# Kernel tuning notes

Measured on AMD Instinct MI355X. Metric: run time of the kernel, lower is better.

## Reference

```python
import jax, jax.numpy as jnp
from jax import lax
import numpy as np

N = 256              # total neurons
EPG_LO, EPG_HI = 0, 64      # epg population slice
PEN_LO, PEN_HI = 64, 128    # pen population slice (two hemispheres of 32)
HEMI = 32                    # hemisphere_length_penalty = len(pen)/2
T = 512              # Euler integration steps
B = 1024             # batch of independent trajectories
DT = 0.01            # integration step (seconds)
TAU0 = 0.02          # default time constant (seconds)


def setup_inputs() -> dict:
    key = jax.random.key(0)
    k_w, k_v, k_l = jax.random.split(key, 3)
    W = jax.random.normal(k_w, (N, N), dtype=jnp.float32) * 0.1
    log_scale = jnp.zeros((), dtype=jnp.float32)          # exp(0)=1, initial_weight_scale=1.0
    gain = jnp.ones((N,), dtype=jnp.float32)              # per-neuron gain mask (exp of per-pop params)
    bias = jnp.zeros((N,), dtype=jnp.float32)
    log_tau = jnp.full((N,), np.log(TAU0), dtype=jnp.float32)  # exp -> tau = 0.02
    velocity_scaling = jnp.float32(0.1)
    landmark_scaling = jnp.float32(0.1)
    velocity = jax.random.normal(k_v, (T, B, 2), dtype=jnp.float32)
    landmarks = jax.random.uniform(k_l, (T, B, EPG_HI - EPG_LO), dtype=jnp.float32)
    return {"W": W, "log_scale": log_scale, "gain": gain, "bias": bias,
            "log_tau": log_tau, "velocity_scaling": velocity_scaling,
            "landmark_scaling": landmark_scaling, "velocity": velocity,
            "landmarks": landmarks}


def reference(W, log_scale, gain, bias, log_tau, velocity_scaling,
              landmark_scaling, velocity, landmarks):
    # Effective recurrent weights: sum over blocks of exp(scale)*masked block
    # collapses to exp(log_scale) * W when all block scalings are tied.
    W_eff = jnp.exp(log_scale) * W                      # [N, N]
    tau = jnp.exp(log_tau)                              # [N]
    coef = DT / tau                                     # [N] Euler dt/tau

    def step(state, xs):                                # state: [B, N]
        v, lm = xs                                      # v: [B, 2], lm: [B, 64]
        ext = jnp.zeros((B, N), dtype=state.dtype)
        # landmark input -> epg neurons
        ext = ext.at[:, EPG_LO:EPG_HI].set(lm * landmark_scaling)
        # angular velocity -> pen neurons, split by hemisphere
        ext = ext.at[:, PEN_LO:PEN_LO + HEMI].set(v[:, :1] * velocity_scaling)
        ext = ext.at[:, PEN_LO + HEMI:PEN_HI].set(v[:, 1:2] * velocity_scaling)
        total = state @ W_eff + ext                     # [B, N]
        rate = jax.nn.relu(gain * total + bias)
        new_state = state + coef * (rate - state)       # leaky Euler update
        return new_state, None

    state0 = jnp.zeros((B, N), dtype=jnp.float32)
    final, _ = lax.scan(step, state0, (velocity, landmarks))
    return final[:, EPG_LO:EPG_HI]                      # epg output, [B, 64]
```

## Files before the change

### kernel.cpp

```cpp
#include <hip/hip_runtime.h>

#define NN 256
#define TT 512
#define BB 1024
#define DTC 0.01f

typedef _Float16 half8 __attribute__((ext_vector_type(8)));
typedef float f32x4 __attribute__((ext_vector_type(4)));
typedef float f32x2 __attribute__((ext_vector_type(2)));

__device__ __forceinline__ f32x4 mfma_z(half8 a, half8 b) {
  f32x4 d;
  asm volatile("v_mfma_f32_16x16x32_f16 %0, %1, %2, 0" : "=v"(d) : "a"(a), "v"(b));
  return d;
}
__device__ __forceinline__ void mfma_p(f32x4& c, half8 a, half8 b) {
  asm volatile("v_mfma_f32_16x16x32_f16 %0, %1, %2, %0" : "+v"(c) : "a"(a), "v"(b));
}

template <int CTRL>
__device__ __forceinline__ float rormax(float x) {
  int yi = __builtin_amdgcn_update_dpp(0, __float_as_int(x), CTRL, 0xf, 0xf, false);
  return fmaxf(x, __int_as_float(yi));
}

__global__ __launch_bounds__(256, 1) void ring_attractor_kernel(
    const float* __restrict__ W, const float* __restrict__ log_scale,
    const float* __restrict__ gain, const float* __restrict__ bias,
    const float* __restrict__ log_tau, const float* __restrict__ vscale_p,
    const float* __restrict__ lscale_p, const float* __restrict__ velocity,
    const float* __restrict__ landmarks, float* __restrict__ out) {
  __shared__ __align__(16) _Float16 fragH[2][4096];
  __shared__ __align__(16) _Float16 fragL[2][4096];
  __shared__ __align__(16) float maxslot[2][4];

  const int tid = threadIdx.x;
  const int w  = tid >> 6;
  const int l  = tid & 63;
  const int g  = l >> 4;
  const int li = l & 15;
  const int br = blockIdx.x * 16 + li;

  const float es  = expf(log_scale[0]);
  const float vs  = vscale_p[0];
  const float lms = lscale_p[0];

  float gain_r[4][4], bias_r[4][4], coef_r[4][4];
#pragma unroll
  for (int nt = 0; nt < 4; ++nt)
#pragma unroll
    for (int q = 0; q < 4; ++q) {
      int c = w * 64 + nt * 16 + g * 4 + q;
      gain_r[nt][q] = gain[c];
      bias_r[nt][q] = bias[c];
      coef_r[nt][q] = DTC / expf(log_tau[c]);
    }

  half8 whi[4][8], wlo[4][8];
#pragma unroll
  for (int nt = 0; nt < 4; ++nt)
#pragma unroll
    for (int ks = 0; ks < 8; ++ks) {
      half8 hi, lo;
#pragma unroll
      for (int j = 0; j < 8; ++j) {
        int k = ks * 32 + g * 4 + (j & 3) + ((j >> 2) << 4);
        int m = w * 64 + nt * 16 + li;
        float wv = W[k * NN + m] * es;
        _Float16 h = (_Float16)wv;
        hi[j] = h;
        lo[j] = (_Float16)(wv - (float)h);
      }
      whi[nt][ks] = hi;
      wlo[nt][ks] = lo;
    }

  float s_r[4][4];
#pragma unroll
  for (int nt = 0; nt < 4; ++nt)
#pragma unroll
    for (int q = 0; q < 4; ++q) s_r[nt][q] = 0.f;

  const int wb0 = ((w * 2 + 0) * 64 + g * 16 + li) * 8;
  const int wb1 = ((w * 2 + 1) * 64 + g * 16 + li) * 8;
  {
    half8 z;
#pragma unroll
    for (int j = 0; j < 8; ++j) z[j] = (_Float16)0.f;
    *reinterpret_cast<half8*>(&fragH[0][wb0]) = z;
    *reinterpret_cast<half8*>(&fragH[0][wb1]) = z;
    *reinterpret_cast<half8*>(&fragL[0][wb0]) = z;
    *reinterpret_cast<half8*>(&fragL[0][wb1]) = z;
    if (tid < 8) maxslot[tid >> 2][tid & 3] = 0.f;
  }
  float inv_scale = 1.f;
  float amPrev = 0.f;
  __syncthreads();

#define RD2(CUR, KS, BH, BL)                                                   \
  {                                                                            \
    const int rb = ((KS)*64 + g * 16 + li) * 8;                                \
    BH = *reinterpret_cast<const half8*>(&fragH[CUR][rb]);                     \
    BL = *reinterpret_cast<const half8*>(&fragL[CUR][rb]);                     \
  }

#define M3Z(AH, AL, AC, NT, BH, BL)                                            \
  AH = mfma_z(whi[NT][0], BH);                                                 \
  AL = mfma_z(wlo[NT][0], BH);                                                 \
  AC = mfma_z(whi[NT][0], BL);

#define M3(AH, AL, AC, NT, KS, BH, BL)                                         \
  mfma_p(AH, whi[NT][KS], BH);                                                 \
  mfma_p(AL, wlo[NT][KS], BH);                                                 \
  mfma_p(AC, whi[NT][KS], BL);

#define TIE0(AH, AL, AC) \
  asm volatile("" : "+v"(AH), "+v"(AL), "+v"(AC))
#define TIEN(AH, AL, AC) \
  asm volatile("s_nop 7\n\ts_nop 7" : "+v"(AH), "+v"(AL), "+v"(AC))

#define TQ(NT, Q, AH, AL, AC)                                                  \
  {                                                                            \
    float av = AH[Q] + AL[Q] + AC[Q];                                          \
    float ext;                                                                 \
    if (w == 0)                                                                \
      ext = lms * ((NT == 0)   ? lm0[Q]                                        \
                   : (NT == 1) ? lm1[Q]                                        \
                   : (NT == 2) ? lm2[Q]                                        \
                               : lm3[Q]);                                      \
    else if (w == 1)                                                           \
      ext = vs * ((NT < 2) ? vv0 : vv1);                                       \
    else                                                                       \
      ext = 0.f;                                                               \
    float tot = __builtin_fmaf(av, inv_scale, ext);                            \
    float rate =                                                               \
        fmaxf(__builtin_fmaf(gain_r[NT][Q], tot, bias_r[NT][Q]), 0.f);         \
    float sv = s_r[NT][Q];                                                     \
    sv = __builtin_fmaf(coef_r[NT][Q], rate - sv, sv);                         \
    s_r[NT][Q] = sv;                                                           \
    am = fmaxf(am, fabsf(sv));                                                 \
  }

#define QHALF(CUR, NTA, NTB, WBX)                                              \
  {                                                                            \
    half8 hq, lq;                                                              \
    _Pragma("unroll") for (int j = 0; j < 4; ++j) {                            \
      float sca = s_r[NTA][j] * scale_n;                                       \
      float scb = s_r[NTB][j] * scale_n;                                       \
      _Float16 qa = (_Float16)sca;                                             \
      _Float16 qb = (_Float16)scb;                                             \
      hq[j] = qa;                                                              \
      lq[j] = (_Float16)(sca - (float)qa);                                     \
      hq[4 + j] = qb;                                                          \
      lq[4 + j] = (_Float16)(scb - (float)qb);                                 \
    }                                                                          \
    *reinterpret_cast<half8*>(&fragH[CUR ^ 1][WBX]) = hq;                      \
    *reinterpret_cast<half8*>(&fragL[CUR ^ 1][WBX]) = lq;                      \
  }

#define STEP(T, CUR)                                                           \
  {                                                                            \
             \
    f32x4 lm0{}, lm1{}, lm2{}, lm3{};                                          \
    float vv0 = 0.f, vv1 = 0.f;                                                \
    if (w == 0) {                                                              \
      const float* p = landmarks + ((size_t)(T)*BB + br) * 64 + g * 4;         \
      lm0 = *reinterpret_cast<const f32x4*>(p);                                \
      lm1 = *reinterpret_cast<const f32x4*>(p + 16);                           \
      lm2 = *reinterpret_cast<const f32x4*>(p + 32);                           \
      lm3 = *reinterpret_cast<const f32x4*>(p + 48);                           \
    } else if (w == 1) {                                                       \
      f32x2 pv = *reinterpret_cast<const f32x2*>(velocity +                    \
                                                 ((size_t)(T)*BB + br) * 2);   \
      vv0 = pv[0];                                                             \
      vv1 = pv[1];                                                             \
    }                                                                          \
                \
    f32x4 mv = *reinterpret_cast<const f32x4*>(&maxslot[CUR ^ 1][0]);          \
                       \
    {                                                                          \
      float r = amPrev;                                                        \
      r = rormax<0x121>(r);                                                    \
      r = rormax<0x122>(r);                                                    \
      r = rormax<0x124>(r);                                                    \
      r = rormax<0x128>(r);                                                    \
      r = fmaxf(r, __shfl_xor(r, 16));                                         \
      r = fmaxf(r, __shfl_xor(r, 32));                                         \
      if (l == 0) maxslot[CUR][w] = r;                                         \
    }                                                                          \
    float scale_n, inv_n;                                                      \
    {                                                                          \
      float M = fmaxf(fmaxf(mv[0], mv[1]), fmaxf(mv[2], mv[3]));               \
      int e = 134 - (int)(__float_as_uint(M) >> 23);                           \
      e = e > 9 ? 9 : e;                                                       \
      scale_n = __int_as_float((e + 127) << 23);                               \
      inv_n = __int_as_float((127 - e) << 23);                                 \
    }                                                                          \
    half8 bh0, bl0, bh1, bl1, bh2, bl2, bh3, bl3;                              \
    half8 bh4, bl4, bh5, bl5, bh6, bl6, bh7, bl7;                              \
    RD2(CUR, 0, bh0, bl0)                                                      \
    RD2(CUR, 1, bh1, bl1)                                                      \
    RD2(CUR, 2, bh2, bl2)                                                      \
    RD2(CUR, 3, bh3, bl3)                                                      \
    RD2(CUR, 4, bh4, bl4)                                                      \
    RD2(CUR, 5, bh5, bl5)                                                      \
    RD2(CUR, 6, bh6, bl6)                                                      \
    RD2(CUR, 7, bh7, bl7)                                                      \
    f32x4 a0h, a0l, a0c, a1h, a1l, a1c, a2h, a2l, a2c, a3h, a3l, a3c;          \
    float am = 0.f;                                                            \
                                                \
    M3Z(a0h, a0l, a0c, 0, bh0, bl0)                                            \
    M3(a0h, a0l, a0c, 0, 1, bh1, bl1)                                          \
    M3(a0h, a0l, a0c, 0, 2, bh2, bl2)                                          \
    M3(a0h, a0l, a0c, 0, 3, bh3, bl3)                                          \
    M3(a0h, a0l, a0c, 0, 4, bh4, bl4)                                          \
    M3(a0h, a0l, a0c, 0, 5, bh5, bl5)                                          \
    M3(a0h, a0l, a0c, 0, 6, bh6, bl6)                                          \
    M3(a0h, a0l, a0c, 0, 7, bh7, bl7)                                          \
         \
    M3Z(a1h, a1l, a1c, 1, bh0, bl0)                                            \
    M3(a1h, a1l, a1c, 1, 1, bh1, bl1)                                          \
    TIE0(a0h, a0l, a0c);                                                       \
    TQ(0, 0, a0h, a0l, a0c)                                                    \
    M3(a1h, a1l, a1c, 1, 2, bh2, bl2)                                          \
    M3(a1h, a1l, a1c, 1, 3, bh3, bl3)                                          \
    TQ(0, 1, a0h, a0l, a0c)                                                    \
    M3(a1h, a1l, a1c, 1, 4, bh4, bl4)                                          \
    M3(a1h, a1l, a1c, 1, 5, bh5, bl5)                                          \
    TQ(0, 2, a0h, a0l, a0c)                                                    \
    M3(a1h, a1l, a1c, 1, 6, bh6, bl6)                                          \
    M3(a1h, a1l, a1c, 1, 7, bh7, bl7)                                          \
    TQ(0, 3, a0h, a0l, a0c)                                                    \
                                          \
    M3Z(a2h, a2l, a2c, 2, bh0, bl0)                                            \
    M3(a2h, a2l, a2c, 2, 1, bh1, bl1)                                          \
    TIE0(a1h, a1l, a1c);                                                       \
    TQ(1, 0, a1h, a1l, a1c)                                                    \
    M3(a2h, a2l, a2c, 2, 2, bh2, bl2)                                          \
    M3(a2h, a2l, a2c, 2, 3, bh3, bl3)                                          \
    TQ(1, 1, a1h, a1l, a1c)                                                    \
    M3(a2h, a2l, a2c, 2, 4, bh4, bl4)                                          \
    M3(a2h, a2l, a2c, 2, 5, bh5, bl5)                                          \
    TQ(1, 2, a1h, a1l, a1c)                                                    \
    M3(a2h, a2l, a2c, 2, 6, bh6, bl6)                                          \
    M3(a2h, a2l, a2c, 2, 7, bh7, bl7)                                          \
    TQ(1, 3, a1h, a1l, a1c)                                                    \
                    \
    M3Z(a3h, a3l, a3c, 3, bh0, bl0)                                            \
    M3(a3h, a3l, a3c, 3, 1, bh1, bl1)                                          \
    QHALF(CUR, 0, 1, wb0)                                                      \
    M3(a3h, a3l, a3c, 3, 2, bh2, bl2)                                          \
    M3(a3h, a3l, a3c, 3, 3, bh3, bl3)                                          \
    TIE0(a2h, a2l, a2c);                                                       \
    TQ(2, 0, a2h, a2l, a2c)                                                    \
    M3(a3h, a3l, a3c, 3, 4, bh4, bl4)                                          \
    M3(a3h, a3l, a3c, 3, 5, bh5, bl5)                                          \
    TQ(2, 1, a2h, a2l, a2c)                                                    \
    M3(a3h, a3l, a3c, 3, 6, bh6, bl6)                                          \
    M3(a3h, a3l, a3c, 3, 7, bh7, bl7)                                          \
    TQ(2, 2, a2h, a2l, a2c)                                                    \
         \
    TQ(2, 3, a2h, a2l, a2c)                                                    \
    TIEN(a3h, a3l, a3c);                                                       \
    TQ(3, 0, a3h, a3l, a3c)                                                    \
    TQ(3, 1, a3h, a3l, a3c)                                                    \
    TQ(3, 2, a3h, a3l, a3c)                                                    \
    TQ(3, 3, a3h, a3l, a3c)                                                    \
    QHALF(CUR, 2, 3, wb1)                                                      \
    amPrev = am;                                                               \
    inv_scale = inv_n;                                                         \
    __syncthreads();                                                           \
  }

#pragma unroll 1
  for (int t = 0; t < TT; t += 2) {
    STEP(t, 0)
    STEP(t + 1, 1)
  }
#undef STEP
#undef QHALF
#undef TQ
#undef TIE0
#undef TIEN
#undef M3
#undef M3Z
#undef RD2

  if (w == 0) {
#pragma unroll
    for (int nt = 0; nt < 4; ++nt) {
      f32x4 o;
#pragma unroll
      for (int q = 0; q < 4; ++q) o[q] = s_r[nt][q];
      *reinterpret_cast<f32x4*>(out + (size_t)br * 64 + nt * 16 + g * 4) = o;
    }
  }
}

extern "C" void kernel_launch(void* const* d_in, const int* in_sizes, int n_in,
                              void* d_out, int out_size, void* d_ws, size_t ws_size,
                              hipStream_t stream) {
  const float* W         = (const float*)d_in[0];
  const float* log_scale = (const float*)d_in[1];
  const float* gain      = (const float*)d_in[2];
  const float* bias      = (const float*)d_in[3];
  const float* log_tau   = (const float*)d_in[4];
  const float* vscale    = (const float*)d_in[5];
  const float* lscale    = (const float*)d_in[6];
  const float* velocity  = (const float*)d_in[7];
  const float* landmarks = (const float*)d_in[8];
  float* out = (float*)d_out;

  ring_attractor_kernel<<<dim3(BB / 16), dim3(256), 0, stream>>>(
      W, log_scale, gain, bias, log_tau, vscale, lscale, velocity, landmarks, out);
}
```

Measured before the change: 794.7 us.

## Split neuron columns across eight waves per block with interleaved MFMA schedule

Doubles the block to 512 threads so each of eight wavefronts owns 32 output neurons instead of 64. This halves per-wave weight registers and MFMA chain length per time step. The MFMA sequence now interleaves the two column tiles with the LDS fragment reads, separated by scheduling barriers. The aim is to shorten the serial per-step critical path in the recurrent loop, at the cost of more waves contending at the per-step barrier and a larger max-reduction slot array.

```diff
diff --git a/kernel.cpp b/kernel.cpp
--- a/kernel.cpp
+++ b/kernel.cpp
@@ -24,7 +24,7 @@
   return fmaxf(x, __int_as_float(yi));
 }
 
-__global__ __launch_bounds__(256, 1) void ring_attractor_kernel(
+__global__ __launch_bounds__(512, 2) void ring_attractor_kernel(
     const float* __restrict__ W, const float* __restrict__ log_scale,
     const float* __restrict__ gain, const float* __restrict__ bias,
     const float* __restrict__ log_tau, const float* __restrict__ vscale_p,
@@ -32,7 +32,7 @@
     const float* __restrict__ landmarks, float* __restrict__ out) {
   __shared__ __align__(16) _Float16 fragH[2][4096];
   __shared__ __align__(16) _Float16 fragL[2][4096];
-  __shared__ __align__(16) float maxslot[2][4];
+  __shared__ __align__(16) float maxslot[2][8];
 
   const int tid = threadIdx.x;
   const int w  = tid >> 6;
@@ -45,27 +45,27 @@
   const float vs  = vscale_p[0];
   const float lms = lscale_p[0];
 
-  float gain_r[4][4], bias_r[4][4], coef_r[4][4];
-#pragma unroll
-  for (int nt = 0; nt < 4; ++nt)
+  float gain_r[2][4], bias_r[2][4], coef_r[2][4];
+#pragma unroll
+  for (int nt = 0; nt < 2; ++nt)
 #pragma unroll
     for (int q = 0; q < 4; ++q) {
-      int c = w * 64 + nt * 16 + g * 4 + q;
+      int c = w * 32 + nt * 16 + g * 4 + q;
       gain_r[nt][q] = gain[c];
       bias_r[nt][q] = bias[c];
       coef_r[nt][q] = DTC / expf(log_tau[c]);
     }
 
-  half8 whi[4][8], wlo[4][8];
-#pragma unroll
-  for (int nt = 0; nt < 4; ++nt)
+  half8 whi[2][8], wlo[2][8];
+#pragma unroll
+  for (int nt = 0; nt < 2; ++nt)
 #pragma unroll
     for (int ks = 0; ks < 8; ++ks) {
       half8 hi, lo;
 #pragma unroll
       for (int j = 0; j < 8; ++j) {
         int k = ks * 32 + g * 4 + (j & 3) + ((j >> 2) << 4);
-        int m = w * 64 + nt * 16 + li;
+        int m = w * 32 + nt * 16 + li;
         float wv = W[k * NN + m] * es;
         _Float16 h = (_Float16)wv;
         hi[j] = h;
@@ -75,27 +75,26 @@
       wlo[nt][ks] = lo;
     }
 
-  float s_r[4][4];
-#pragma unroll
-  for (int nt = 0; nt < 4; ++nt)
+  float s_r[2][4];
+#pragma unroll
+  for (int nt = 0; nt < 2; ++nt)
 #pragma unroll
     for (int q = 0; q < 4; ++q) s_r[nt][q] = 0.f;
 
-  const int wb0 = ((w * 2 + 0) * 64 + g * 16 + li) * 8;
-  const int wb1 = ((w * 2 + 1) * 64 + g * 16 + li) * 8;
+  const int wb = (w * 64 + g * 16 + li) * 8;
   {
     half8 z;
 #pragma unroll
     for (int j = 0; j < 8; ++j) z[j] = (_Float16)0.f;
-    *reinterpret_cast<half8*>(&fragH[0][wb0]) = z;
-    *reinterpret_cast<half8*>(&fragH[0][wb1]) = z;
-    *reinterpret_cast<half8*>(&fragL[0][wb0]) = z;
-    *reinterpret_cast<half8*>(&fragL[0][wb1]) = z;
-    if (tid < 8) maxslot[tid >> 2][tid & 3] = 0.f;
+    *reinterpret_cast<half8*>(&fragH[0][wb]) = z;
+    *reinterpret_cast<half8*>(&fragL[0][wb]) = z;
+    if (tid < 16) maxslot[tid >> 3][tid & 7] = 0.f;
   }
   float inv_scale = 1.f;
   float amPrev = 0.f;
   __syncthreads();
+
+#define SB() __builtin_amdgcn_sched_barrier(0)
 
 #define RD2(CUR, KS, BH, BL)                                                   \
   {                                                                            \
@@ -104,18 +103,21 @@
     BL = *reinterpret_cast<const half8*>(&fragL[CUR][rb]);                     \
   }
 
-#define M3Z(AH, AL, AC, NT, BH, BL)                                            \
-  AH = mfma_z(whi[NT][0], BH);                                                 \
-  AL = mfma_z(wlo[NT][0], BH);                                                 \
-  AC = mfma_z(whi[NT][0], BL);
-
-#define M3(AH, AL, AC, NT, KS, BH, BL)                                         \
-  mfma_p(AH, whi[NT][KS], BH);                                                 \
-  mfma_p(AL, wlo[NT][KS], BH);                                                 \
-  mfma_p(AC, whi[NT][KS], BL);
-
-#define TIE0(AH, AL, AC) \
-  asm volatile("" : "+v"(AH), "+v"(AL), "+v"(AC))
+#define K6Z(BH, BL)                                                            \
+  a0h = mfma_z(whi[0][0], BH);                                                 \
+  a1h = mfma_z(whi[1][0], BH);                                                 \
+  a0l = mfma_z(wlo[0][0], BH);                                                 \
+  a1l = mfma_z(wlo[1][0], BH);                                                 \
+  a0c = mfma_z(whi[0][0], BL);                                                 \
+  a1c = mfma_z(whi[1][0], BL);
+#define K6(KS, BH, BL)                                                         \
+  mfma_p(a0h, whi[0][KS], BH);                                                 \
+  mfma_p(a1h, whi[1][KS], BH);                                                 \
+  mfma_p(a0l, wlo[0][KS], BH);                                                 \
+  mfma_p(a1l, wlo[1][KS], BH);                                                 \
+  mfma_p(a0c, whi[0][KS], BL);                                                 \
+  mfma_p(a1c, whi[1][KS], BL);
+
 #define TIEN(AH, AL, AC) \
   asm volatile("s_nop 7\n\ts_nop 7" : "+v"(AH), "+v"(AL), "+v"(AC))
 
@@ -123,13 +125,12 @@
   {                                                                            \
     float av = AH[Q] + AL[Q] + AC[Q];                                          \
     float ext;                                                                 \
-    if (w == 0)                                                                \
-      ext = lms * ((NT == 0)   ? lm0[Q]                                        \
-                   : (NT == 1) ? lm1[Q]                                        \
-                   : (NT == 2) ? lm2[Q]                                        \
-                               : lm3[Q]);                                      \
-    else if (w == 1)                                                           \
-      ext = vs * ((NT < 2) ? vv0 : vv1);                                       \
+    if (w < 2)                                                                 \
+      ext = lms * ((NT) ? lm1[Q] : lm0[Q]);                                    \
+    else if (w == 2)                                                           \
+      ext = vs * vv0;                                                          \
+    else if (w == 3)                                                           \
+      ext = vs * vv1;                                                          \
     else                                                                       \
       ext = 0.f;                                                               \
     float tot = __builtin_fmaf(av, inv_scale, ext);                            \
@@ -141,43 +142,24 @@
     am = fmaxf(am, fabsf(sv));                                                 \
   }
 
-#define QHALF(CUR, NTA, NTB, WBX)                                              \
-  {                                                                            \
-    half8 hq, lq;                                                              \
-    _Pragma("unroll") for (int j = 0; j < 4; ++j) {                            \
-      float sca = s_r[NTA][j] * scale_n;                                       \
-      float scb = s_r[NTB][j] * scale_n;                                       \
-      _Float16 qa = (_Float16)sca;                                             \
-      _Float16 qb = (_Float16)scb;                                             \
-      hq[j] = qa;                                                              \
-      lq[j] = (_Float16)(sca - (float)qa);                                     \
-      hq[4 + j] = qb;                                                          \
-      lq[4 + j] = (_Float16)(scb - (float)qb);                                 \
-    }                                                                          \
-    *reinterpret_cast<half8*>(&fragH[CUR ^ 1][WBX]) = hq;                      \
-    *reinterpret_cast<half8*>(&fragL[CUR ^ 1][WBX]) = lq;                      \
-  }
-
 #define STEP(T, CUR)                                                           \
   {                                                                            \
-             \
-    f32x4 lm0{}, lm1{}, lm2{}, lm3{};                                          \
+                           \
+    f32x4 lm0{}, lm1{};                                                        \
     float vv0 = 0.f, vv1 = 0.f;                                                \
-    if (w == 0) {                                                              \
-      const float* p = landmarks + ((size_t)(T)*BB + br) * 64 + g * 4;         \
+    if (w < 2) {                                                               \
+      const float* p = landmarks + ((size_t)(T)*BB + br) * 64 + w * 32 + g * 4;\
       lm0 = *reinterpret_cast<const f32x4*>(p);                                \
       lm1 = *reinterpret_cast<const f32x4*>(p + 16);                           \
-      lm2 = *reinterpret_cast<const f32x4*>(p + 32);                           \
-      lm3 = *reinterpret_cast<const f32x4*>(p + 48);                           \
-    } else if (w == 1) {                                                       \
+    } else if (w < 4) {                                                        \
       f32x2 pv = *reinterpret_cast<const f32x2*>(velocity +                    \
                                                  ((size_t)(T)*BB + br) * 2);   \
       vv0 = pv[0];                                                             \
       vv1 = pv[1];                                                             \
     }                                                                          \
-                \
-    f32x4 mv = *reinterpret_cast<const f32x4*>(&maxslot[CUR ^ 1][0]);          \
-                       \
+                 \
+    f32x4 mva = *reinterpret_cast<const f32x4*>(&maxslot[CUR ^ 1][0]);         \
+    f32x4 mvb = *reinterpret_cast<const f32x4*>(&maxslot[CUR ^ 1][4]);         \
     {                                                                          \
       float r = amPrev;                                                        \
       r = rormax<0x121>(r);                                                    \
@@ -190,83 +172,70 @@
     }                                                                          \
     float scale_n, inv_n;                                                      \
     {                                                                          \
-      float M = fmaxf(fmaxf(mv[0], mv[1]), fmaxf(mv[2], mv[3]));               \
+      float M = fmaxf(fmaxf(fmaxf(mva[0], mva[1]), fmaxf(mva[2], mva[3])),     \
+                      fmaxf(fmaxf(mvb[0], mvb[1]), fmaxf(mvb[2], mvb[3])));    \
       int e = 134 - (int)(__float_as_uint(M) >> 23);                           \
       e = e > 9 ? 9 : e;                                                       \
       scale_n = __int_as_float((e + 127) << 23);                               \
       inv_n = __int_as_float((127 - e) << 23);                                 \
     }                                                                          \
+                   \
     half8 bh0, bl0, bh1, bl1, bh2, bl2, bh3, bl3;                              \
     half8 bh4, bl4, bh5, bl5, bh6, bl6, bh7, bl7;                              \
+    f32x4 a0h, a0l, a0c, a1h, a1l, a1c;                                        \
     RD2(CUR, 0, bh0, bl0)                                                      \
     RD2(CUR, 1, bh1, bl1)                                                      \
+    SB();                                                                      \
+    K6Z(bh0, bl0)                                                              \
+    SB();                                                                      \
     RD2(CUR, 2, bh2, bl2)                                                      \
+    SB();                                                                      \
+    K6(1, bh1, bl1)                                                            \
+    SB();                                                                      \
     RD2(CUR, 3, bh3, bl3)                                                      \
+    SB();                                                                      \
+    K6(2, bh2, bl2)                                                            \
+    SB();                                                                      \
     RD2(CUR, 4, bh4, bl4)                                                      \
+    SB();                                                                      \
+    K6(3, bh3, bl3)                                                            \
+    SB();                                                                      \
     RD2(CUR, 5, bh5, bl5)                                                      \
+    SB();                                                                      \
+    K6(4, bh4, bl4)                                                            \
+    SB();                                                                      \
     RD2(CUR, 6, bh6, bl6)                                                      \
+    SB();                                                                      \
+    K6(5, bh5, bl5)                                                            \
+    SB();                                                                      \
     RD2(CUR, 7, bh7, bl7)                                                      \
-    f32x4 a0h, a0l, a0c, a1h, a1l, a1c, a2h, a2l, a2c, a3h, a3l, a3c;          \
+    SB();                                                                      \
+    K6(6, bh6, bl6)                                                            \
+    K6(7, bh7, bl7)                                                            \
+              \
     float am = 0.f;                                                            \
-                                                \
-    M3Z(a0h, a0l, a0c, 0, bh0, bl0)                                            \
-    M3(a0h, a0l, a0c, 0, 1, bh1, bl1)                                          \
-    M3(a0h, a0l, a0c, 0, 2, bh2, bl2)                                          \
-    M3(a0h, a0l, a0c, 0, 3, bh3, bl3)                                          \
-    M3(a0h, a0l, a0c, 0, 4, bh4, bl4)                                          \
-    M3(a0h, a0l, a0c, 0, 5, bh5, bl5)                                          \
-    M3(a0h, a0l, a0c, 0, 6, bh6, bl6)                                          \
-    M3(a0h, a0l, a0c, 0, 7, bh7, bl7)                                          \
-         \
-    M3Z(a1h, a1l, a1c, 1, bh0, bl0)                                            \
-    M3(a1h, a1l, a1c, 1, 1, bh1, bl1)                                          \
-    TIE0(a0h, a0l, a0c);                                                       \
+    TIEN(a0h, a0l, a0c);                                                       \
     TQ(0, 0, a0h, a0l, a0c)                                                    \
-    M3(a1h, a1l, a1c, 1, 2, bh2, bl2)                                          \
-    M3(a1h, a1l, a1c, 1, 3, bh3, bl3)                                          \
     TQ(0, 1, a0h, a0l, a0c)                                                    \
-    M3(a1h, a1l, a1c, 1, 4, bh4, bl4)                                          \
-    M3(a1h, a1l, a1c, 1, 5, bh5, bl5)                                          \
     TQ(0, 2, a0h, a0l, a0c)                                                    \
-    M3(a1h, a1l, a1c, 1, 6, bh6, bl6)                                          \
-    M3(a1h, a1l, a1c, 1, 7, bh7, bl7)                                          \
     TQ(0, 3, a0h, a0l, a0c)                                                    \
-                                          \
-    M3Z(a2h, a2l, a2c, 2, bh0, bl0)                                            \
-    M3(a2h, a2l, a2c, 2, 1, bh1, bl1)                                          \
-    TIE0(a1h, a1l, a1c);                                                       \
+    TIEN(a1h, a1l, a1c);                                                       \
     TQ(1, 0, a1h, a1l, a1c)                                                    \
-    M3(a2h, a2l, a2c, 2, 2, bh2, bl2)                                          \
-    M3(a2h, a2l, a2c, 2, 3, bh3, bl3)                                          \
     TQ(1, 1, a1h, a1l, a1c)                                                    \
-    M3(a2h, a2l, a2c, 2, 4, bh4, bl4)                                          \
-    M3(a2h, a2l, a2c, 2, 5, bh5, bl5)                                          \
     TQ(1, 2, a1h, a1l, a1c)                                                    \
-    M3(a2h, a2l, a2c, 2, 6, bh6, bl6)                                          \
-    M3(a2h, a2l, a2c, 2, 7, bh7, bl7)                                          \
     TQ(1, 3, a1h, a1l, a1c)                                                    \
-                    \
-    M3Z(a3h, a3l, a3c, 3, bh0, bl0)                                            \
-    M3(a3h, a3l, a3c, 3, 1, bh1, bl1)                                          \
-    QHALF(CUR, 0, 1, wb0)                                                      \
-    M3(a3h, a3l, a3c, 3, 2, bh2, bl2)                                          \
-    M3(a3h, a3l, a3c, 3, 3, bh3, bl3)                                          \
-    TIE0(a2h, a2l, a2c);                                                       \
-    TQ(2, 0, a2h, a2l, a2c)                                                    \
-    M3(a3h, a3l, a3c, 3, 4, bh4, bl4)                                          \
-    M3(a3h, a3l, a3c, 3, 5, bh5, bl5)                                          \
-    TQ(2, 1, a2h, a2l, a2c)                                                    \
-    M3(a3h, a3l, a3c, 3, 6, bh6, bl6)                                          \
-    M3(a3h, a3l, a3c, 3, 7, bh7, bl7)                                          \
-    TQ(2, 2, a2h, a2l, a2c)                                                    \
-         \
-    TQ(2, 3, a2h, a2l, a2c)                                                    \
-    TIEN(a3h, a3l, a3c);                                                       \
-    TQ(3, 0, a3h, a3l, a3c)                                                    \
-    TQ(3, 1, a3h, a3l, a3c)                                                    \
-    TQ(3, 2, a3h, a3l, a3c)                                                    \
-    TQ(3, 3, a3h, a3l, a3c)                                                    \
-    QHALF(CUR, 2, 3, wb1)                                                      \
+                   \
+    {                                                                          \
+      half8 hq, lq;                                                            \
+      _Pragma("unroll") for (int j = 0; j < 8; ++j) {                          \
+        float sc = s_r[j >> 2][j & 3] * scale_n;                               \
+        _Float16 qh = (_Float16)sc;                                            \
+        hq[j] = qh;                                                            \
+        lq[j] = (_Float16)(sc - (float)qh);                                    \
+      }                                                                        \
+      *reinterpret_cast<half8*>(&fragH[CUR ^ 1][wb]) = hq;                     \
+      *reinterpret_cast<half8*>(&fragL[CUR ^ 1][wb]) = lq;                     \
+    }                                                                          \
     amPrev = am;                                                               \
     inv_scale = inv_n;                                                         \
     __syncthreads();                                                           \
@@ -278,21 +247,21 @@
     STEP(t + 1, 1)
   }
 #undef STEP
-#undef QHALF
 #undef TQ
-#undef TIE0
 #undef TIEN
-#undef M3
-#undef M3Z
+#undef K6
+#undef K6Z
 #undef RD2
-
-  if (w == 0) {
-#pragma unroll
-    for (int nt = 0; nt < 4; ++nt) {
+#undef SB
+
+  if (w < 2) {
+#pragma unroll
+    for (int nt = 0; nt < 2; ++nt) {
       f32x4 o;
 #pragma unroll
       for (int q = 0; q < 4; ++q) o[q] = s_r[nt][q];
-      *reinterpret_cast<f32x4*>(out + (size_t)br * 64 + nt * 16 + g * 4) = o;
+      *reinterpret_cast<f32x4*>(out + (size_t)br * 64 + w * 32 + nt * 16 +
+                                g * 4) = o;
     }
   }
 }
@@ -311,6 +280,6 @@
   const float* landmarks = (const float*)d_in[8];
   float* out = (float*)d_out;
 
-  ring_attractor_kernel<<<dim3(BB / 16), dim3(256), 0, stream>>>(
+  ring_attractor_kernel<<<dim3(BB / 16), dim3(512), 0, stream>>>(
       W, log_scale, gain, bias, log_tau, vscale, lscale, velocity, landmarks, out);
 }
```

Result: slower. 962.2 us (+21.1%).
